# Kernel optimization log

Hardware: AMD Instinct MI355X
Metric: run time of the kernel (lower is better)

## Reference

```python
import jax, jax.numpy as jnp
import numpy as np

N_HEADS = 4
N_HIDDEN = 64  # out_features (concat=False)
MASK_FILL = -9e15
ADJ_THRESH = 0.05


def setup_inputs() -> dict:
    key = jax.random.key(0)
    k1, k2, k3, k4 = jax.random.split(key, 4)
    B, S, N, F = 32, 20, 128, 64
    h = jax.random.normal(k1, (B, S, N, F), dtype=jnp.float32)
    adj_mat = jax.random.uniform(k2, (B, S, N, N), dtype=jnp.float32)
    W = jax.random.normal(k3, (F, N_HEADS * N_HIDDEN), dtype=jnp.float32) * (1.0 / np.sqrt(F))
    a = jax.random.normal(k4, (N_HEADS, 2 * N_HIDDEN, 1), dtype=jnp.float32) * 0.1
    return {"h": h, "adj_mat": adj_mat, "W": W, "a": a}


def reference(h, adj_mat, W, a):
    B, S, N, _ = h.shape
    # Linear projection (no bias); dropout is a no-op (training=False)
    ht = jnp.einsum('bsnf,fo->bsno', h, W)
    # (B, S, H, N, D)
    ht = ht.reshape(B, S, N, N_HEADS, N_HIDDEN).transpose(0, 1, 3, 2, 4)
    a_src = a[:, :N_HIDDEN, 0]   # (H, D)
    a_tgt = a[:, N_HIDDEN:, 0]   # (H, D)
    src = jnp.einsum('bshnd,hd->bshn', ht, a_src)  # (B,S,H,N)
    tgt = jnp.einsum('bshnd,hd->bshn', ht, a_tgt)
    # additive sigmoid score: e_ij = sigmoid(src_i + tgt_j)
    e = jax.nn.sigmoid(src[..., :, None] + tgt[..., None, :])  # (B,S,H,N,N)
    mask = (adj_mat < ADJ_THRESH)[:, :, None, :, :]  # broadcast over heads
    e = jnp.where(mask, MASK_FILL, e)
    attn = jax.nn.softmax(e, axis=-1)
    h_prime = jnp.einsum('bshij,bshjd->bshid', attn, ht)
    # concat=False -> mean over heads
    return h_prime.mean(axis=2)  # (B,S,N,D)
```

## Files before the change

### kernel.cpp

```cpp
#include <hip/hip_runtime.h>
#include <hip/hip_bf16.h>

#define ADJ_TH 0.05f

typedef __bf16 bf16x8 __attribute__((ext_vector_type(8)));
typedef __bf16 bf16x4 __attribute__((ext_vector_type(4)));
typedef float  f32x4  __attribute__((ext_vector_type(4)));

__global__ void wt_convert_kernel(const float* __restrict__ W, __bf16* __restrict__ Wt) {
    int id = blockIdx.x * 256 + threadIdx.x;
    int o = id >> 6, k = id & 63;
    Wt[o * 64 + k] = (__bf16)W[k * 256 + o];
}

__device__ __forceinline__ int sw_idx(int o, int i) {
    return o * 128 + ((((i >> 3) ^ o) & 15) << 3) + (i & 7);
}

__global__ __launch_bounds__(256, 2)
void gat_main_kernel(const float* __restrict__ hg, const float* __restrict__ adj,
                     const float* __restrict__ ag, const __bf16* __restrict__ Wt,
                     float* __restrict__ out)
{
    const int bs  = blockIdx.x;
    const int tid = threadIdx.x;
    const int w   = tid >> 6;
    const int l   = tid & 63;
    const int l15 = l & 15;
    const int l4  = l >> 4;

    __shared__ __bf16   ht_t[256 * 128];
    __shared__ float    srctgt[1024];
    __shared__ float    a_sh[512];
    __shared__ unsigned mask_sh[512];

    const float* hb = hg  + (size_t)bs * 128 * 64;
    const float* ab = adj + (size_t)bs * 128 * 128;

    a_sh[tid]       = ag[tid];
    a_sh[tid + 256] = ag[tid + 256];

    #pragma unroll
    for (int rp = 0; rp < 2; ++rp) {
        int widx = tid + rp * 256;
        int i = widx >> 2, wq = widx & 3;
        const float4* ap = reinterpret_cast<const float4*>(ab + i * 128 + wq * 32);
        unsigned bits = 0u;
        #pragma unroll
        for (int v = 0; v < 8; ++v) {
            float4 f = ap[v];
            bits |= (f.x < ADJ_TH ? 1u : 0u) << (4 * v + 0);
            bits |= (f.y < ADJ_TH ? 1u : 0u) << (4 * v + 1);
            bits |= (f.z < ADJ_TH ? 1u : 0u) << (4 * v + 2);
            bits |= (f.w < ADJ_TH ? 1u : 0u) << (4 * v + 3);
        }
        mask_sh[i * 4 + wq] = bits;
    }

    {
        bf16x8 af[2][2];
        #pragma unroll
        for (int m2 = 0; m2 < 2; ++m2) {
            int row = 16 * (2 * w + m2) + l15;
            #pragma unroll
            for (int ks = 0; ks < 2; ++ks) {
                const float4* p4 = reinterpret_cast<const float4*>(hb + row * 64 + 8 * l4 + 32 * ks);
                float4 lo = p4[0], hi = p4[1];
                bf16x8 v;
                v[0] = (__bf16)lo.x; v[1] = (__bf16)lo.y; v[2] = (__bf16)lo.z; v[3] = (__bf16)lo.w;
                v[4] = (__bf16)hi.x; v[5] = (__bf16)hi.y; v[6] = (__bf16)hi.z; v[7] = (__bf16)hi.w;
                af[m2][ks] = v;
            }
        }
        #pragma unroll
        for (int nt = 0; nt < 16; ++nt) {
            int o = 16 * nt + l15;
            bf16x8 bf0 = *reinterpret_cast<const bf16x8*>(Wt + o * 64 + 8 * l4);
            bf16x8 bf1 = *reinterpret_cast<const bf16x8*>(Wt + o * 64 + 8 * l4 + 32);
            #pragma unroll
            for (int m2 = 0; m2 < 2; ++m2) {
                f32x4 acc = {0.f, 0.f, 0.f, 0.f};
                acc = __builtin_amdgcn_mfma_f32_16x16x32_bf16(af[m2][0], bf0, acc, 0, 0, 0);
                acc = __builtin_amdgcn_mfma_f32_16x16x32_bf16(af[m2][1], bf1, acc, 0, 0, 0);
                int i0 = 16 * (2 * w + m2) + 4 * l4;
                bf16x4 st;
                st[0] = (__bf16)acc[0]; st[1] = (__bf16)acc[1];
                st[2] = (__bf16)acc[2]; st[3] = (__bf16)acc[3];
                *reinterpret_cast<bf16x4*>(&ht_t[sw_idx(o, i0)]) = st;
            }
        }
    }
    __syncthreads();

    #pragma unroll
    for (int rp = 0; rp < 2; ++rp) {
        int p = tid + rp * 256;
        int hh = p >> 7, i = p & 127;
        float s = 0.f, g = 0.f;
        #pragma unroll
        for (int d = 0; d < 64; ++d) {
            float v = (float)ht_t[sw_idx(hh * 64 + d, i)];
            s += v * a_sh[hh * 128 + d];
            g += v * a_sh[hh * 128 + 64 + d];
        }
        srctgt[hh * 128 + i]       = s;
        srctgt[512 + hh * 128 + i] = g;
    }
    __syncthreads();

    f32x4 acc2[2][4];
    #pragma unroll
    for (int m2 = 0; m2 < 2; ++m2)
        #pragma unroll
        for (int nt = 0; nt < 4; ++nt) {
            f32x4 z = {0.f, 0.f, 0.f, 0.f};
            acc2[m2][nt] = z;
        }

    #pragma unroll 1
    for (int hd = 0; hd < 4; ++hd) {
        bf16x8 bfr[4][4];
        #pragma unroll
        for (int nt = 0; nt < 4; ++nt)
            #pragma unroll
            for (int ks = 0; ks < 4; ++ks)
                bfr[nt][ks] = *reinterpret_cast<const bf16x8*>(
                    &ht_t[sw_idx(64 * hd + 16 * nt + l15, 8 * l4 + 32 * ks)]);

        float tg[4][8];
        #pragma unroll
        for (int ks = 0; ks < 4; ++ks) {
            const float4* tp = reinterpret_cast<const float4*>(&srctgt[512 + hd * 128 + 8 * l4 + 32 * ks]);
            float4 t0 = tp[0], t1 = tp[1];
            tg[ks][0] = t0.x; tg[ks][1] = t0.y; tg[ks][2] = t0.z; tg[ks][3] = t0.w;
            tg[ks][4] = t1.x; tg[ks][5] = t1.y; tg[ks][6] = t1.z; tg[ks][7] = t1.w;
        }

        #pragma unroll
        for (int m2 = 0; m2 < 2; ++m2) {
            int irow = 16 * (2 * w + m2) + l15;
            float si = srctgt[hd * 128 + irow];
            unsigned mw[4];
            #pragma unroll
            for (int ks = 0; ks < 4; ++ks) mw[ks] = mask_sh[irow * 4 + ks];

            float pf[4][8];
            float dloc = 0.f;
            #pragma unroll
            for (int ks = 0; ks < 4; ++ks)
                #pragma unroll
                for (int e = 0; e < 8; ++e) {
                    float x  = si + tg[ks][e];
                    float sg = __builtin_amdgcn_rcpf(1.0f + __expf(-x));
                    float pe = __expf(sg);
                    float p  = ((mw[ks] >> (8 * l4 + e)) & 1u) ? 0.f : pe;
                    pf[ks][e] = p;
                    dloc += p;
                }
            dloc += __shfl_xor(dloc, 16);
            dloc += __shfl_xor(dloc, 32);
            float scale = 0.25f * __builtin_amdgcn_rcpf(fmaxf(dloc, 1e-20f));

            bf16x8 pa[4];
            #pragma unroll
            for (int ks = 0; ks < 4; ++ks) {
                bf16x8 v;
                #pragma unroll
                for (int e = 0; e < 8; ++e) v[e] = (__bf16)(pf[ks][e] * scale);
                pa[ks] = v;
            }
            #pragma unroll
            for (int nt = 0; nt < 4; ++nt) {
                f32x4 acc = acc2[m2][nt];
                #pragma unroll
                for (int ks = 0; ks < 4; ++ks)
                    acc = __builtin_amdgcn_mfma_f32_16x16x32_bf16(pa[ks], bfr[nt][ks], acc, 0, 0, 0);
                acc2[m2][nt] = acc;
            }
        }
    }

    float* ob = out + (size_t)bs * 128 * 64;
    #pragma unroll
    for (int m2 = 0; m2 < 2; ++m2)
        #pragma unroll
        for (int nt = 0; nt < 4; ++nt)
            #pragma unroll
            for (int r = 0; r < 4; ++r)
                ob[(32 * w + 16 * m2 + 4 * l4 + r) * 64 + 16 * nt + l15] = acc2[m2][nt][r];
}

extern "C" void kernel_launch(void* const* d_in, const int* in_sizes, int n_in,
                              void* d_out, int out_size, void* d_ws, size_t ws_size,
                              hipStream_t stream) {
    const float* h   = (const float*)d_in[0];
    const float* adj = (const float*)d_in[1];
    const float* W   = (const float*)d_in[2];
    const float* a   = (const float*)d_in[3];
    float* out = (float*)d_out;
    __bf16* Wt = (__bf16*)d_ws;

    wt_convert_kernel<<<64, 256, 0, stream>>>(W, Wt);
    gat_main_kernel<<<640, 256, 0, stream>>>(h, adj, a, Wt, out);
}
```

Baseline: 143.5 us.

## Process heads in pairs to halve LDS, fuse src/tgt into projection, split mask build

The main kernel now projects and attends two heads at a time. The ht_t LDS buffer shrinks from 64KB to 32KB so launch bounds can ask for 4 blocks per CU instead of 2. The src/tgt attention scores are computed inside the projection MFMA epilogue with shuffle reductions, replacing the separate LDS pass. The adjacency bitmask is built by a separate kernel into workspace and loaded as uint4 per row, falling back to in-kernel construction if the workspace is too small. The extra kernel launch and the global mask round trip are added in exchange, and capping registers for 4 blocks per CU may cause spills.

```diff
diff --git a/kernel.cpp b/kernel.cpp
--- a/kernel.cpp
+++ b/kernel.cpp
@@ -13,14 +13,37 @@
     Wt[o * 64 + k] = (__bf16)W[k * 256 + o];
 }
 
+__global__ __launch_bounds__(256)
+void mask_build_kernel(const float* __restrict__ adj, unsigned* __restrict__ mws) {
+    int bs = blockIdx.x, tid = threadIdx.x;
+    const float* ab = adj + (size_t)bs * 128 * 128;
+    #pragma unroll
+    for (int rp = 0; rp < 2; ++rp) {
+        int widx = tid + rp * 256;
+        int i = widx >> 2, wq = widx & 3;
+        const float4* ap = reinterpret_cast<const float4*>(ab + i * 128 + wq * 32);
+        unsigned bits = 0u;
+        #pragma unroll
+        for (int v = 0; v < 8; ++v) {
+            float4 f = ap[v];
+            bits |= (f.x < ADJ_TH ? 1u : 0u) << (4 * v + 0);
+            bits |= (f.y < ADJ_TH ? 1u : 0u) << (4 * v + 1);
+            bits |= (f.z < ADJ_TH ? 1u : 0u) << (4 * v + 2);
+            bits |= (f.w < ADJ_TH ? 1u : 0u) << (4 * v + 3);
+        }
+        mws[(bs * 128 + i) * 4 + wq] = bits;
+    }
+}
+
 __device__ __forceinline__ int sw_idx(int o, int i) {
     return o * 128 + ((((i >> 3) ^ o) & 15) << 3) + (i & 7);
 }
 
-__global__ __launch_bounds__(256, 2)
+template<bool WSMASK>
+__global__ __launch_bounds__(256, 4)
 void gat_main_kernel(const float* __restrict__ hg, const float* __restrict__ adj,
                      const float* __restrict__ ag, const __bf16* __restrict__ Wt,
-                     float* __restrict__ out)
+                     const unsigned* __restrict__ mws, float* __restrict__ out)
 {
     const int bs  = blockIdx.x;
     const int tid = threadIdx.x;
@@ -29,35 +52,47 @@
     const int l15 = l & 15;
     const int l4  = l >> 4;
 
-    __shared__ __bf16   ht_t[256 * 128];
-    __shared__ float    srctgt[1024];
-    __shared__ float    a_sh[512];
-    __shared__ unsigned mask_sh[512];
-
-    const float* hb = hg  + (size_t)bs * 128 * 64;
-    const float* ab = adj + (size_t)bs * 128 * 128;
-
-    a_sh[tid]       = ag[tid];
-    a_sh[tid + 256] = ag[tid + 256];
-
+    __shared__ __bf16   ht_t[128 * 128];
+    __shared__ float    src_sh[2][128], tgt_sh[2][128];
+    __shared__ unsigned mask_sh[WSMASK ? 4 : 512];
+
+    const float* hb = hg + (size_t)bs * 128 * 64;
+
+    uint4 mq[2];
+    if constexpr (WSMASK) {
+        #pragma unroll
+        for (int m2 = 0; m2 < 2; ++m2) {
+            int irow = 16 * (2 * w + m2) + l15;
+            mq[m2] = *reinterpret_cast<const uint4*>(mws + ((size_t)bs * 128 + irow) * 4);
+        }
+    } else {
+        const float* ab = adj + (size_t)bs * 128 * 128;
+        #pragma unroll
+        for (int rp = 0; rp < 2; ++rp) {
+            int widx = tid + rp * 256;
+            int i = widx >> 2, wq = widx & 3;
+            const float4* ap = reinterpret_cast<const float4*>(ab + i * 128 + wq * 32);
+            unsigned bits = 0u;
+            #pragma unroll
+            for (int v = 0; v < 8; ++v) {
+                float4 f = ap[v];
+                bits |= (f.x < ADJ_TH ? 1u : 0u) << (4 * v + 0);
+                bits |= (f.y < ADJ_TH ? 1u : 0u) << (4 * v + 1);
+                bits |= (f.z < ADJ_TH ? 1u : 0u) << (4 * v + 2);
+                bits |= (f.w < ADJ_TH ? 1u : 0u) << (4 * v + 3);
+            }
+            mask_sh[i * 4 + wq] = bits;
+        }
+    }
+
+    f32x4 acc2[2][4];
     #pragma unroll
-    for (int rp = 0; rp < 2; ++rp) {
-        int widx = tid + rp * 256;
-        int i = widx >> 2, wq = widx & 3;
-        const float4* ap = reinterpret_cast<const float4*>(ab + i * 128 + wq * 32);
-        unsigned bits = 0u;
-        #pragma unroll
-        for (int v = 0; v < 8; ++v) {
-            float4 f = ap[v];
-            bits |= (f.x < ADJ_TH ? 1u : 0u) << (4 * v + 0);
-            bits |= (f.y < ADJ_TH ? 1u : 0u) << (4 * v + 1);
-            bits |= (f.z < ADJ_TH ? 1u : 0u) << (4 * v + 2);
-            bits |= (f.w < ADJ_TH ? 1u : 0u) << (4 * v + 3);
-        }
-        mask_sh[i * 4 + wq] = bits;
-    }
-
-    {
+    for (int m2 = 0; m2 < 2; ++m2)
+        #pragma unroll
+        for (int nt = 0; nt < 4; ++nt) { f32x4 z = {0.f,0.f,0.f,0.f}; acc2[m2][nt] = z; }
+
+    #pragma unroll 1
+    for (int p = 0; p < 2; ++p) {
         bf16x8 af[2][2];
         #pragma unroll
         for (int m2 = 0; m2 < 2; ++m2) {
@@ -67,117 +102,137 @@
                 const float4* p4 = reinterpret_cast<const float4*>(hb + row * 64 + 8 * l4 + 32 * ks);
                 float4 lo = p4[0], hi = p4[1];
                 bf16x8 v;
-                v[0] = (__bf16)lo.x; v[1] = (__bf16)lo.y; v[2] = (__bf16)lo.z; v[3] = (__bf16)lo.w;
-                v[4] = (__bf16)hi.x; v[5] = (__bf16)hi.y; v[6] = (__bf16)hi.z; v[7] = (__bf16)hi.w;
+                v[0]=(__bf16)lo.x; v[1]=(__bf16)lo.y; v[2]=(__bf16)lo.z; v[3]=(__bf16)lo.w;
+                v[4]=(__bf16)hi.x; v[5]=(__bf16)hi.y; v[6]=(__bf16)hi.z; v[7]=(__bf16)hi.w;
                 af[m2][ks] = v;
             }
         }
-        #pragma unroll
-        for (int nt = 0; nt < 16; ++nt) {
-            int o = 16 * nt + l15;
-            bf16x8 bf0 = *reinterpret_cast<const bf16x8*>(Wt + o * 64 + 8 * l4);
-            bf16x8 bf1 = *reinterpret_cast<const bf16x8*>(Wt + o * 64 + 8 * l4 + 32);
+
+        #pragma unroll
+        for (int hg2 = 0; hg2 < 2; ++hg2) {
+            int h = 2 * p + hg2;
+            float ps[2][4], pt[2][4];
+            #pragma unroll
+            for (int m2 = 0; m2 < 2; ++m2)
+                #pragma unroll
+                for (int r = 0; r < 4; ++r) { ps[m2][r] = 0.f; pt[m2][r] = 0.f; }
+
+            #pragma unroll
+            for (int nq = 0; nq < 4; ++nq) {
+                int nt   = 4 * hg2 + nq;
+                int oloc = 16 * nt + l15;
+                int og   = 128 * p + oloc;
+                int d    = 16 * nq + l15;
+                float a_s = ag[h * 128 + d];
+                float a_t = ag[h * 128 + 64 + d];
+                bf16x8 b0 = *reinterpret_cast<const bf16x8*>(Wt + og * 64 + 8 * l4);
+                bf16x8 b1 = *reinterpret_cast<const bf16x8*>(Wt + og * 64 + 8 * l4 + 32);
+                #pragma unroll
+                for (int m2 = 0; m2 < 2; ++m2) {
+                    f32x4 acc = {0.f,0.f,0.f,0.f};
+                    acc = __builtin_amdgcn_mfma_f32_16x16x32_bf16(af[m2][0], b0, acc, 0,0,0);
+                    acc = __builtin_amdgcn_mfma_f32_16x16x32_bf16(af[m2][1], b1, acc, 0,0,0);
+                    int i0 = 16 * (2 * w + m2) + 4 * l4;
+                    bf16x4 st;
+                    st[0]=(__bf16)acc[0]; st[1]=(__bf16)acc[1];
+                    st[2]=(__bf16)acc[2]; st[3]=(__bf16)acc[3];
+                    *reinterpret_cast<bf16x4*>(&ht_t[sw_idx(oloc, i0)]) = st;
+                    #pragma unroll
+                    for (int r = 0; r < 4; ++r) {
+                        ps[m2][r] += acc[r] * a_s;
+                        pt[m2][r] += acc[r] * a_t;
+                    }
+                }
+            }
+            #pragma unroll
+            for (int s = 1; s < 16; s <<= 1)
+                #pragma unroll
+                for (int m2 = 0; m2 < 2; ++m2)
+                    #pragma unroll
+                    for (int r = 0; r < 4; ++r) {
+                        ps[m2][r] += __shfl_xor(ps[m2][r], s);
+                        pt[m2][r] += __shfl_xor(pt[m2][r], s);
+                    }
+            if (l15 == 0) {
+                #pragma unroll
+                for (int m2 = 0; m2 < 2; ++m2)
+                    #pragma unroll
+                    for (int r = 0; r < 4; ++r) {
+                        int i = 16 * (2 * w + m2) + 4 * l4 + r;
+                        src_sh[hg2][i] = ps[m2][r];
+                        tgt_sh[hg2][i] = pt[m2][r];
+                    }
+            }
+        }
+        __syncthreads();
+
+        #pragma unroll 1
+        for (int hp = 0; hp < 2; ++hp) {
+            bf16x8 bfr[4][4];
+            #pragma unroll
+            for (int nt = 0; nt < 4; ++nt)
+                #pragma unroll
+                for (int ks = 0; ks < 4; ++ks)
+                    bfr[nt][ks] = *reinterpret_cast<const bf16x8*>(
+                        &ht_t[sw_idx(64 * hp + 16 * nt + l15, 8 * l4 + 32 * ks)]);
+
+            float tg[4][8];
+            #pragma unroll
+            for (int ks = 0; ks < 4; ++ks) {
+                const float4* tp = reinterpret_cast<const float4*>(&tgt_sh[hp][8 * l4 + 32 * ks]);
+                float4 t0 = tp[0], t1 = tp[1];
+                tg[ks][0]=t0.x; tg[ks][1]=t0.y; tg[ks][2]=t0.z; tg[ks][3]=t0.w;
+                tg[ks][4]=t1.x; tg[ks][5]=t1.y; tg[ks][6]=t1.z; tg[ks][7]=t1.w;
+            }
+
             #pragma unroll
             for (int m2 = 0; m2 < 2; ++m2) {
-                f32x4 acc = {0.f, 0.f, 0.f, 0.f};
-                acc = __builtin_amdgcn_mfma_f32_16x16x32_bf16(af[m2][0], bf0, acc, 0, 0, 0);
-                acc = __builtin_amdgcn_mfma_f32_16x16x32_bf16(af[m2][1], bf1, acc, 0, 0, 0);
-                int i0 = 16 * (2 * w + m2) + 4 * l4;
-                bf16x4 st;
-                st[0] = (__bf16)acc[0]; st[1] = (__bf16)acc[1];
-                st[2] = (__bf16)acc[2]; st[3] = (__bf16)acc[3];
-                *reinterpret_cast<bf16x4*>(&ht_t[sw_idx(o, i0)]) = st;
-            }
-        }
-    }
-    __syncthreads();
-
-    #pragma unroll
-    for (int rp = 0; rp < 2; ++rp) {
-        int p = tid + rp * 256;
-        int hh = p >> 7, i = p & 127;
-        float s = 0.f, g = 0.f;
-        #pragma unroll
-        for (int d = 0; d < 64; ++d) {
-            float v = (float)ht_t[sw_idx(hh * 64 + d, i)];
-            s += v * a_sh[hh * 128 + d];
-            g += v * a_sh[hh * 128 + 64 + d];
-        }
-        srctgt[hh * 128 + i]       = s;
-        srctgt[512 + hh * 128 + i] = g;
-    }
-    __syncthreads();
-
-    f32x4 acc2[2][4];
-    #pragma unroll
-    for (int m2 = 0; m2 < 2; ++m2)
-        #pragma unroll
-        for (int nt = 0; nt < 4; ++nt) {
-            f32x4 z = {0.f, 0.f, 0.f, 0.f};
-            acc2[m2][nt] = z;
-        }
-
-    #pragma unroll 1
-    for (int hd = 0; hd < 4; ++hd) {
-        bf16x8 bfr[4][4];
-        #pragma unroll
-        for (int nt = 0; nt < 4; ++nt)
-            #pragma unroll
-            for (int ks = 0; ks < 4; ++ks)
-                bfr[nt][ks] = *reinterpret_cast<const bf16x8*>(
-                    &ht_t[sw_idx(64 * hd + 16 * nt + l15, 8 * l4 + 32 * ks)]);
-
-        float tg[4][8];
-        #pragma unroll
-        for (int ks = 0; ks < 4; ++ks) {
-            const float4* tp = reinterpret_cast<const float4*>(&srctgt[512 + hd * 128 + 8 * l4 + 32 * ks]);
-            float4 t0 = tp[0], t1 = tp[1];
-            tg[ks][0] = t0.x; tg[ks][1] = t0.y; tg[ks][2] = t0.z; tg[ks][3] = t0.w;
-            tg[ks][4] = t1.x; tg[ks][5] = t1.y; tg[ks][6] = t1.z; tg[ks][7] = t1.w;
-        }
-
-        #pragma unroll
-        for (int m2 = 0; m2 < 2; ++m2) {
-            int irow = 16 * (2 * w + m2) + l15;
-            float si = srctgt[hd * 128 + irow];
-            unsigned mw[4];
-            #pragma unroll
-            for (int ks = 0; ks < 4; ++ks) mw[ks] = mask_sh[irow * 4 + ks];
-
-            float pf[4][8];
-            float dloc = 0.f;
-            #pragma unroll
-            for (int ks = 0; ks < 4; ++ks)
-                #pragma unroll
-                for (int e = 0; e < 8; ++e) {
-                    float x  = si + tg[ks][e];
-                    float sg = __builtin_amdgcn_rcpf(1.0f + __expf(-x));
-                    float pe = __expf(sg);
-                    float p  = ((mw[ks] >> (8 * l4 + e)) & 1u) ? 0.f : pe;
-                    pf[ks][e] = p;
-                    dloc += p;
-                }
-            dloc += __shfl_xor(dloc, 16);
-            dloc += __shfl_xor(dloc, 32);
-            float scale = 0.25f * __builtin_amdgcn_rcpf(fmaxf(dloc, 1e-20f));
-
-            bf16x8 pa[4];
-            #pragma unroll
-            for (int ks = 0; ks < 4; ++ks) {
-                bf16x8 v;
-                #pragma unroll
-                for (int e = 0; e < 8; ++e) v[e] = (__bf16)(pf[ks][e] * scale);
-                pa[ks] = v;
-            }
-            #pragma unroll
-            for (int nt = 0; nt < 4; ++nt) {
-                f32x4 acc = acc2[m2][nt];
+                int irow = 16 * (2 * w + m2) + l15;
+                float si = src_sh[hp][irow];
+                unsigned mw[4];
+                if constexpr (WSMASK) {
+                    mw[0]=mq[m2].x; mw[1]=mq[m2].y; mw[2]=mq[m2].z; mw[3]=mq[m2].w;
+                } else {
+                    uint4 t = *reinterpret_cast<const uint4*>(&mask_sh[irow * 4]);
+                    mw[0]=t.x; mw[1]=t.y; mw[2]=t.z; mw[3]=t.w;
+                }
+
+                float pf[4][8];
+                float dloc = 0.f;
                 #pragma unroll
                 for (int ks = 0; ks < 4; ++ks)
-                    acc = __builtin_amdgcn_mfma_f32_16x16x32_bf16(pa[ks], bfr[nt][ks], acc, 0, 0, 0);
-                acc2[m2][nt] = acc;
-            }
-        }
+                    #pragma unroll
+                    for (int e = 0; e < 8; ++e) {
+                        float x  = si + tg[ks][e];
+                        float sg = __builtin_amdgcn_rcpf(1.0f + __expf(-x));
+                        float pe = __expf(sg);
+                        float pv = ((mw[ks] >> (8 * l4 + e)) & 1u) ? 0.f : pe;
+                        pf[ks][e] = pv;
+                        dloc += pv;
+                    }
+                dloc += __shfl_xor(dloc, 16);
+                dloc += __shfl_xor(dloc, 32);
+                float scale = 0.25f * __builtin_amdgcn_rcpf(fmaxf(dloc, 1e-20f));
+
+                bf16x8 pa[4];
+                #pragma unroll
+                for (int ks = 0; ks < 4; ++ks) {
+                    bf16x8 v;
+                    #pragma unroll
+                    for (int e = 0; e < 8; ++e) v[e] = (__bf16)(pf[ks][e] * scale);
+                    pa[ks] = v;
+                }
+                #pragma unroll
+                for (int nt = 0; nt < 4; ++nt) {
+                    f32x4 acc = acc2[m2][nt];
+                    #pragma unroll
+                    for (int ks = 0; ks < 4; ++ks)
+                        acc = __builtin_amdgcn_mfma_f32_16x16x32_bf16(pa[ks], bfr[nt][ks], acc, 0,0,0);
+                    acc2[m2][nt] = acc;
+                }
+            }
+        }
+        __syncthreads();
     }
 
     float* ob = out + (size_t)bs * 128 * 64;
@@ -198,8 +253,16 @@
     const float* W   = (const float*)d_in[2];
     const float* a   = (const float*)d_in[3];
     float* out = (float*)d_out;
-    __bf16* Wt = (__bf16*)d_ws;
+
+    __bf16*   Wt  = (__bf16*)d_ws;
+    unsigned* mws = (unsigned*)((char*)d_ws + 65536);
+    const size_t need = 65536 + (size_t)640 * 128 * 4 * sizeof(unsigned);
 
     wt_convert_kernel<<<64, 256, 0, stream>>>(W, Wt);
-    gat_main_kernel<<<640, 256, 0, stream>>>(h, adj, a, Wt, out);
-}
+    if (ws_size >= need) {
+        mask_build_kernel<<<640, 256, 0, stream>>>(adj, mws);
+        gat_main_kernel<true><<<640, 256, 0, stream>>>(h, adj, a, Wt, mws, out);
+    } else {
+        gat_main_kernel<false><<<640, 256, 0, stream>>>(h, adj, a, Wt, mws, out);
+    }
+}
```

Result: slower. 169.6 us (+18.2%).
